# Kernel tuning notes

Measured on AMD Instinct MI355X. Metric: run time of the kernel, lower is better.

Reference implementation:

```python
import jax, jax.numpy as jnp
import numpy as np

EPS = 1e-5
B, CIN, L = 512, 5, 1024   # batch, input channels, msp length == d_model
COUT, A, NB = 32, 13, 5    # CNN branch channels, max_atoms, num_bonds_prediction


def conv1d(x, w, pad, groups=1):
    # x: (N, C, L), w: (O, I/groups, K)
    return jax.lax.conv_general_dilated(
        x, w, window_strides=(1,), padding=[(pad, pad)],
        dimension_numbers=("NCH", "OIH", "NCH"), feature_group_count=groups)


def batchnorm(x, g, b):
    # training-mode BN over (N, L) per channel, as nn.BatchNorm1d in train()
    m = jnp.mean(x, axis=(0, 2), keepdims=True)
    v = jnp.var(x, axis=(0, 2), keepdims=True)
    return (x - m) * jax.lax.rsqrt(v + EPS) * g[None, :, None] + b[None, :, None]


def setup_inputs() -> dict:
    key = jax.random.key(0)
    ks = jax.random.split(key, 16)
    n = jax.random.normal
    inp = {
        "src": n(ks[0], (B, CIN, L), dtype=jnp.float32),
        "mask": jnp.ones((B, A), dtype=bool),
        "max_atoms": A,
        # CNN branch 1 (kernel 5) : depthwise, pointwise, BN, residual 1x1 conv
        "dw1": n(ks[1], (CIN, 1, 5), dtype=jnp.float32) * 0.2,
        "pw1": n(ks[2], (COUT, CIN, 1), dtype=jnp.float32) * 0.2,
        "g1": jnp.ones((COUT,), jnp.float32),
        "be1": jnp.zeros((COUT,), jnp.float32),
        "r1w": n(ks[3], (COUT, CIN, 1), dtype=jnp.float32) * 0.2,
        "r1b": jnp.zeros((COUT,), jnp.float32),
        # CNN branch 2 (kernel 3)
        "dw2": n(ks[4], (CIN, 1, 3), dtype=jnp.float32) * 0.2,
        "pw2": n(ks[5], (COUT, CIN, 1), dtype=jnp.float32) * 0.2,
        "g2": jnp.ones((COUT,), jnp.float32),
        "be2": jnp.zeros((COUT,), jnp.float32),
        "r2w": n(ks[6], (COUT, CIN, 1), dtype=jnp.float32) * 0.2,
        "r2b": jnp.zeros((COUT,), jnp.float32),
        # EdgeClassify2 linears: ll1 (2*COUT -> A), fl (2*L -> NB)
        "ll1w": n(ks[7], (A, 2 * COUT), dtype=jnp.float32) * 0.1,
        "ll1b": jnp.zeros((A,), jnp.float32),
        "flw": n(ks[8], (NB, 2 * L), dtype=jnp.float32) * 0.02,
        "flb": jnp.zeros((NB,), jnp.float32),
    }
    return inp


def reference(src, mask, max_atoms, dw1, pw1, g1, be1, r1w, r1b,
              dw2, pw2, g2, be2, r2w, r2b, ll1w, ll1b, flw, flb):
    # ---- CNN encoder ----
    e1 = jax.nn.relu(batchnorm(conv1d(conv1d(src, dw1, 2, groups=CIN), pw1, 0), g1, be1))
    e1 = e1 * (conv1d(src, r1w, 0) + r1b[None, :, None])
    e2 = jax.nn.relu(batchnorm(conv1d(conv1d(src, dw2, 1, groups=CIN), pw2, 0), g2, be2))
    e2 = e2 * (conv1d(src, r2w, 0) + r2b[None, :, None])
    x = jnp.concatenate([e1, e2], axis=1)          # (B, 2*COUT, L)
    # ---- EdgeClassify2 ----
    # ll1 over channel dim: (B, 2*COUT, L) -> (B, A, L)
    h = jnp.einsum("bcl,ac->bal", x, ll1w) + ll1b[None, :, None]
    # vectorized replacement of the O(A^2) python loop:
    # final_e[:, i, j] = concat(h[:, min(i,j)], h[:, max(i,j)])
    idx = jnp.arange(max_atoms)
    mn = jnp.minimum(idx[:, None], idx[None, :])   # (A, A)
    mx = jnp.maximum(idx[:, None], idx[None, :])
    final_e = jnp.concatenate([h[:, mn, :], h[:, mx, :]], axis=-1)  # (B, A, A, 2L)
    out = jnp.einsum("bijd,nd->bijn", final_e, flw) + flb           # (B, A, A, NB)
    return out
```

## Files before the change

kernel.cpp:

```cpp
#include <hip/hip_runtime.h>
#include <hip/hip_bf16.h>

#define BB 512
#define LL 1024
#define AA 13
#define NBP 5
#define NTOT (BB * LL)
#define EPSV 1e-5f

#define WS_F     192
#define WS_PART  256
#define WS_CONST 10496

typedef __attribute__((ext_vector_type(8))) short bhalf8;
typedef __attribute__((ext_vector_type(4))) float floatx4;

template<int CTRL, int RM, bool BC>
__device__ __forceinline__ float dppadd(float v) {
    int t = __builtin_amdgcn_update_dpp(0, __float_as_int(v), CTRL, RM, 0xf, BC);
    return v + __int_as_float(t);
}
__device__ __forceinline__ float wave_sum(float v) {
    v = dppadd<0x111, 0xf, true >(v);
    v = dppadd<0x112, 0xf, true >(v);
    v = dppadd<0x114, 0xf, true >(v);
    v = dppadd<0x118, 0xf, true >(v);
    v = dppadd<0x142, 0xa, false>(v);
    v = dppadd<0x143, 0xc, false>(v);
    return v;
}

__global__ __launch_bounds__(256) void k_moments(
    const float* __restrict__ src,
    const float* __restrict__ dw1,
    const float* __restrict__ dw2,
    const float* __restrict__ flw,
    float* __restrict__ ws)
{
    __shared__ float red[4][40];
    __shared__ float fred[4];
    int tid = threadIdx.x;
    int gid = blockIdx.x * 256 + tid;
    int b = gid >> 7, L0 = (gid & 127) << 3;
    const float* sb = src + b * (5 * LL);

    float w1[5][5], w2[5][3];
#pragma unroll
    for (int c = 0; c < 5; c++) {
#pragma unroll
        for (int t = 0; t < 5; t++) w1[c][t] = dw1[c*5+t];
#pragma unroll
        for (int t = 0; t < 3; t++) w2[c][t] = dw2[c*3+t];
    }

    float x[5][16];
#pragma unroll
    for (int c5 = 0; c5 < 5; c5++) {
        const float* sp = sb + c5 * LL;
        float4 xa = (L0 >= 4)    ? *(const float4*)(sp + L0 - 4) : make_float4(0,0,0,0);
        float4 xb = *(const float4*)(sp + L0);
        float4 xc = *(const float4*)(sp + L0 + 4);
        float4 xd = (L0 <= 1012) ? *(const float4*)(sp + L0 + 8) : make_float4(0,0,0,0);
        x[c5][0]=xa.x; x[c5][1]=xa.y; x[c5][2]=xa.z; x[c5][3]=xa.w;
        x[c5][4]=xb.x; x[c5][5]=xb.y; x[c5][6]=xb.z; x[c5][7]=xb.w;
        x[c5][8]=xc.x; x[c5][9]=xc.y; x[c5][10]=xc.z; x[c5][11]=xc.w;
        x[c5][12]=xd.x; x[c5][13]=xd.y; x[c5][14]=xd.z; x[c5][15]=xd.w;
    }

    float acc[40];
#pragma unroll
    for (int k = 0; k < 40; k++) acc[k] = 0.f;

#pragma unroll
    for (int k = 0; k < 8; k++) {
        float d1[5], d2[5];
#pragma unroll
        for (int c5 = 0; c5 < 5; c5++) {
            d1[c5] = w1[c5][0]*x[c5][k+2] + w1[c5][1]*x[c5][k+3] + w1[c5][2]*x[c5][k+4]
                   + w1[c5][3]*x[c5][k+5] + w1[c5][4]*x[c5][k+6];
            d2[c5] = w2[c5][0]*x[c5][k+3] + w2[c5][1]*x[c5][k+4] + w2[c5][2]*x[c5][k+5];
        }
#pragma unroll
        for (int j = 0; j < 5; j++) { acc[j] += d1[j]; acc[20+j] += d2[j]; }
#pragma unroll
        for (int j = 0; j < 5; j++)
#pragma unroll
            for (int kk = j; kk < 5; kk++) {
                int idx = j*(11-j)/2 + (kk - j);
                acc[5+idx]  += d1[j]*d1[kk];
                acc[25+idx] += d2[j]*d2[kk];
            }
    }

    int lane = tid & 63, wv = tid >> 6;
#pragma unroll
    for (int k = 0; k < 40; k++) acc[k] = wave_sum(acc[k]);
    if (lane == 63) {
#pragma unroll
        for (int k = 0; k < 40; k++) red[wv][k] = acc[k];
    }
    __syncthreads();
    if (tid < 40) {
        ws[WS_PART + blockIdx.x * 40 + tid] =
            red[0][tid] + red[1][tid] + red[2][tid] + red[3][tid];
    }

    if (blockIdx.x < 10) {
        int nn = blockIdx.x;
        int n = nn < 5 ? nn : nn - 5;
        int off = nn < 5 ? 0 : LL;
        float4 v = *(const float4*)(flw + n * (2*LL) + off + tid * 4);
        float s = wave_sum(v.x + v.y + v.z + v.w);
        if (lane == 63) fred[wv] = s;
        __syncthreads();
        if (tid == 0) ws[WS_F + nn] = fred[0] + fred[1] + fred[2] + fred[3];
    }
}

__global__ __launch_bounds__(320) void k_prep(
    float* __restrict__ ws,
    const float* __restrict__ pw1, const float* __restrict__ pw2,
    const float* __restrict__ g1,  const float* __restrict__ be1,
    const float* __restrict__ g2,  const float* __restrict__ be2,
    const float* __restrict__ r1w, const float* __restrict__ r2w,
    const float* __restrict__ r1b, const float* __restrict__ r2b)
{
    __shared__ float momS[40];
    int tid = threadIdx.x;
    {
        int k = tid >> 3, sub = tid & 7;
        float v = 0.f;
#pragma unroll 8
        for (int t2 = 0; t2 < 32; t2++) v += ws[WS_PART + (sub + (t2 << 3)) * 40 + k];
        v += __shfl_xor(v, 1, 64);
        v += __shfl_xor(v, 2, 64);
        v += __shfl_xor(v, 4, 64);
        if (sub == 0) momS[k] = v;
    }
    __syncthreads();
    if (tid < 64) {
        int brc = tid >> 5, o = tid & 31;
        const float invN = 1.0f / (float)NTOT;
        const float* pw = brc ? pw2 : pw1;
        const float* rw = brc ? r2w : r1w;
        const float* s  = momS + (brc ? 20 : 0);
        const float* M  = momS + (brc ? 25 : 5);
        float pwv[5], rwv[5], md[5];
#pragma unroll
        for (int j = 0; j < 5; j++) { pwv[j] = pw[o*5+j]; rwv[j] = rw[o*5+j]; md[j] = s[j] * invN; }
        float meanY = 0.f;
#pragma unroll
        for (int j = 0; j < 5; j++) meanY += pwv[j] * md[j];
        float ey2 = 0.f;
#pragma unroll
        for (int j = 0; j < 5; j++)
#pragma unroll
            for (int k = 0; k < 5; k++) {
                int lo = j < k ? j : k, hi = j < k ? k : j;
                int idx = lo*(11-lo)/2 + (hi - lo);
                ey2 += pwv[j] * pwv[k] * (M[idx] * invN);
            }
        float varY = ey2 - meanY * meanY;
        if (varY < 0.f) varY = 0.f;
        float gg = brc ? g2[o] : g1[o];
        float bb = brc ? be2[o] : be1[o];
        float rb = brc ? r2b[o] : r1b[o];
        float sc = gg * rsqrtf(varY + EPSV);
        float sh = bb - meanY * sc;
        float* dst = ws + WS_CONST + tid * 16;
        dst[0] = pwv[0]*sc; dst[1] = pwv[1]*sc; dst[2] = pwv[2]*sc; dst[3] = pwv[3]*sc;
        dst[4] = pwv[4]*sc; dst[5] = sh;        dst[6] = rb;        dst[7] = 0.f;
        dst[8] = rwv[0];    dst[9] = rwv[1];    dst[10] = rwv[2];   dst[11] = rwv[3];
        dst[12] = rwv[4];   dst[13] = 0.f;      dst[14] = 0.f;      dst[15] = 0.f;
    }
}

__global__ __launch_bounds__(1024, 1) void k_fused(
    const float* __restrict__ src,
    const float* __restrict__ dw1,
    const float* __restrict__ dw2,
    const float* __restrict__ flw,
    const float* __restrict__ ll1w,
    const float* __restrict__ ll1b,
    const float* __restrict__ flb,
    const float* __restrict__ ws,
    float* __restrict__ out)
{
    __shared__ __align__(16) float srcS[5][1040];
    __shared__ float llT[832];
    __shared__ __align__(16) unsigned int eBuf[16384];
    __shared__ __align__(16) float Sarr[1024];
    __shared__ float PQ[130];

    int tid = threadIdx.x, b = blockIdx.x;
    int lane = tid & 63;
    int gu = __builtin_amdgcn_readfirstlane(tid >> 6);
    int br = gu >> 3;
    int c0 = gu << 2;

    const float* srcB = src + b * (5 * LL);

    for (int idx = tid; idx < 5 * 256; idx += 1024) {
        int c5 = idx >> 8, q = idx & 255;
        float4 v = *(const float4*)(srcB + (c5 << 10) + (q << 2));
        *(float4*)&srcS[c5][(q << 2) + 8] = v;
    }
    if (tid < 40) {
        int c5 = tid >> 3, j = tid & 7;
        int i = (j < 4) ? (4 + j) : (1028 + j);
        srcS[c5][i] = 0.f;
    }
    for (int idx = tid; idx < 832; idx += 1024) {
        int cc = idx / 13, a = idx - cc * 13;
        llT[idx] = ll1w[a * 64 + cc];
    }

    float wdw[5][5];
    if (br == 0) {
#pragma unroll
        for (int c5 = 0; c5 < 5; c5++)
#pragma unroll
            for (int t = 0; t < 5; t++) wdw[c5][t] = dw1[c5*5+t];
    } else {
#pragma unroll
        for (int c5 = 0; c5 < 5; c5++) {
            wdw[c5][0] = 0.f;
            wdw[c5][1] = dw2[c5*3+0]; wdw[c5][2] = dw2[c5*3+1]; wdw[c5][3] = dw2[c5*3+2];
            wdw[c5][4] = 0.f;
        }
    }
    const float* cb = ws + WS_CONST + (c0 << 4);

    int mt  = gu & 3;
    int ks0 = (gu >> 2) << 1;
    floatx4 Cacc = {0.f, 0.f, 0.f, 0.f};

    int nB = lane & 15;
    int kg = (lane >> 4) << 3;
    const float* fbase = flw + (nB % 5) * 2048 + (nB / 5) * 1024;

    __syncthreads();

#pragma unroll 1
    for (int p = 0; p < 4; ++p) {
        float fv[2][8];
        {
            int gl0 = (p << 8) + (ks0 << 5) + kg;
            if (nB < 10) {
                float4 a0 = *(const float4*)(fbase + gl0);
                float4 a1 = *(const float4*)(fbase + gl0 + 4);
                float4 b0 = *(const float4*)(fbase + gl0 + 32);
                float4 b1 = *(const float4*)(fbase + gl0 + 36);
                fv[0][0]=a0.x; fv[0][1]=a0.y; fv[0][2]=a0.z; fv[0][3]=a0.w;
                fv[0][4]=a1.x; fv[0][5]=a1.y; fv[0][6]=a1.z; fv[0][7]=a1.w;
                fv[1][0]=b0.x; fv[1][1]=b0.y; fv[1][2]=b0.z; fv[1][3]=b0.w;
                fv[1][4]=b1.x; fv[1][5]=b1.y; fv[1][6]=b1.z; fv[1][7]=b1.w;
            } else {
#pragma unroll
                for (int j = 0; j < 8; j++) { fv[0][j] = 0.f; fv[1][j] = 0.f; }
            }
        }

        int l0 = (p << 8) + (lane << 2);
        float dv[5][4], sv[5][4];
        {
            int i0 = l0 + 8;
#pragma unroll
            for (int c5 = 0; c5 < 5; c5++) {
                float4 xa = *(const float4*)&srcS[c5][i0 - 4];
                float4 xb = *(const float4*)&srcS[c5][i0];
                float4 xc = *(const float4*)&srcS[c5][i0 + 4];
                float xx[12] = {xa.x, xa.y, xa.z, xa.w, xb.x, xb.y, xb.z, xb.w, xc.x, xc.y, xc.z, xc.w};
                sv[c5][0] = xb.x; sv[c5][1] = xb.y; sv[c5][2] = xb.z; sv[c5][3] = xb.w;
                if (br == 0) {
#pragma unroll
                    for (int q = 0; q < 4; q++)
                        dv[c5][q] = wdw[c5][0]*xx[q+2] + wdw[c5][1]*xx[q+3] + wdw[c5][2]*xx[q+4]
                                  + wdw[c5][3]*xx[q+5] + wdw[c5][4]*xx[q+6];
                } else {
#pragma unroll
                    for (int q = 0; q < 4; q++)
                        dv[c5][q] = wdw[c5][1]*xx[q+3] + wdw[c5][2]*xx[q+4] + wdw[c5][3]*xx[q+5];
                }
            }
        }

        char* eb = (char*)eBuf;
#pragma unroll
        for (int ci = 0; ci < 4; ci++) {
            const float4 A  = *(const float4*)(cb + ci*16);
            const float4 B2 = *(const float4*)(cb + ci*16 + 4);
            const float4 R0 = *(const float4*)(cb + ci*16 + 8);
            const float4 R1 = *(const float4*)(cb + ci*16 + 12);
            unsigned int hp[2], lp[2];
#pragma unroll
            for (int hq = 0; hq < 2; hq++) {
                unsigned int hw[2], lw[2];
#pragma unroll
                for (int s = 0; s < 2; s++) {
                    int q = hq * 2 + s;
                    float y = B2.y + A.x*dv[0][q] + A.y*dv[1][q] + A.z*dv[2][q]
                                    + A.w*dv[3][q] + B2.x*dv[4][q];
                    float r = B2.z + R0.x*sv[0][q] + R0.y*sv[1][q] + R0.z*sv[2][q]
                                    + R0.w*sv[3][q] + R1.x*sv[4][q];
                    float e = fmaxf(y, 0.f) * r;
                    unsigned int u = __float_as_uint(e);
                    hw[s] = u & 0xFFFF0000u;
                    float lf = e - __uint_as_float(hw[s]);
                    lw[s] = __float_as_uint(lf) & 0xFFFF0000u;
                }
                hp[hq] = (hw[0] >> 16) | hw[1];
                lp[hq] = (lw[0] >> 16) | lw[1];
            }
            int c = c0 + ci;
            int off = (c << 9) + (((lane << 3)) ^ ((c & 7) << 4));
            *(uint2*)(eb + off)         = make_uint2(hp[0], hp[1]);
            *(uint2*)(eb + 32768 + off) = make_uint2(lp[0], lp[1]);
        }
        __syncthreads();

        {
            int arow = (mt << 4) + (lane & 15);
            int swz  = (arow & 7) << 4;
            int rb2  = arow << 9;
#pragma unroll
            for (int kk = 0; kk < 2; kk++) {
                int ksl = (ks0 + kk) << 5;
                int kbyte = (((ksl + kg) << 1)) ^ swz;
                bhalf8 aH = *(const bhalf8*)(eb + rb2 + kbyte);
                bhalf8 aL = *(const bhalf8*)(eb + 32768 + rb2 + kbyte);
                bhalf8 bH, bL;
#pragma unroll
                for (int j = 0; j < 8; j++) {
                    float f = fv[kk][j];
                    unsigned int u = __float_as_uint(f);
                    unsigned int hu = u & 0xFFFF0000u;
                    bH[j] = (short)(u >> 16);
                    float lf = f - __uint_as_float(hu);
                    bL[j] = (short)(__float_as_uint(lf) >> 16);
                }
                Cacc = __builtin_amdgcn_mfma_f32_16x16x32_bf16(aH, bH, Cacc, 0, 0, 0);
                Cacc = __builtin_amdgcn_mfma_f32_16x16x32_bf16(aH, bL, Cacc, 0, 0, 0);
                Cacc = __builtin_amdgcn_mfma_f32_16x16x32_bf16(aL, bH, Cacc, 0, 0, 0);
            }
        }
        __syncthreads();
    }

    {
        float* part = (float*)eBuf;
        int basep = (gu << 8) + ((lane >> 4) << 6) + (lane & 15);
        part[basep]      = Cacc[0];
        part[basep + 16] = Cacc[1];
        part[basep + 32] = Cacc[2];
        part[basep + 48] = Cacc[3];
    }
    __syncthreads();
    {
        int c = tid >> 4, n = tid & 15;
        int m = c >> 4, row = c & 15;
        const float* part = (const float*)eBuf;
        int o = (row << 4) + n;
        float s = part[(m) * 256 + o] + part[(4 + m) * 256 + o]
                + part[(8 + m) * 256 + o] + part[(12 + m) * 256 + o];
        Sarr[tid] = s;
    }
    __syncthreads();

    if (tid < 130) {
        int half = tid >= 65 ? 1 : 0;
        int q = tid - half * 65;
        int a = q / 5, n = q - a * 5;
        int col = half * 5 + n;
        float v = ll1b[a] * ws[WS_F + col];
#pragma unroll 8
        for (int cc = 0; cc < 64; cc++) v += llT[cc * 13 + a] * Sarr[(cc << 4) + col];
        PQ[tid] = v;
    }
    __syncthreads();

    for (int idx = tid; idx < AA * AA * NBP; idx += 1024) {
        int i = idx / 65;
        int rr = idx - i * 65;
        int j = rr / 5, n = rr - j * 5;
        int mn = i < j ? i : j, mx = i < j ? j : i;
        out[b * (AA * AA * NBP) + idx] = PQ[mn * 5 + n] + PQ[65 + mx * 5 + n] + flb[n];
    }
}

extern "C" void kernel_launch(void* const* d_in, const int* in_sizes, int n_in,
                              void* d_out, int out_size, void* d_ws, size_t ws_size,
                              hipStream_t stream) {
    const float* src  = (const float*)d_in[0];
    const float* dw1  = (const float*)d_in[3];
    const float* pw1  = (const float*)d_in[4];
    const float* g1   = (const float*)d_in[5];
    const float* be1  = (const float*)d_in[6];
    const float* r1w  = (const float*)d_in[7];
    const float* r1b  = (const float*)d_in[8];
    const float* dw2  = (const float*)d_in[9];
    const float* pw2  = (const float*)d_in[10];
    const float* g2   = (const float*)d_in[11];
    const float* be2  = (const float*)d_in[12];
    const float* r2w  = (const float*)d_in[13];
    const float* r2b  = (const float*)d_in[14];
    const float* ll1w = (const float*)d_in[15];
    const float* ll1b = (const float*)d_in[16];
    const float* flw  = (const float*)d_in[17];
    const float* flb  = (const float*)d_in[18];
    float* ws  = (float*)d_ws;
    float* out = (float*)d_out;

    k_moments<<<256, 256, 0, stream>>>(src, dw1, dw2, flw, ws);
    k_prep<<<1, 320, 0, stream>>>(ws, pw1, pw2, g1, be1, g2, be2, r1w, r2w, r1b, r2b);
    k_fused<<<BB, 1024, 0, stream>>>(src, dw1, dw2, flw, ll1w, ll1b, flb, ws, out);
}
```

Measured before the change: 142.4 us.

## Halve shared eBuf by staging hi/lo bf16 halves sequentially for two blocks per CU

The shared staging buffer for the split-bf16 activation tile is halved. The high part is written first and consumed by two MFMAs, then the low part is held in registers, written into the same buffer and consumed by the third MFMA. Launch bounds are raised to allow two 1024-thread blocks per CU. The aim is to cut LDS use so a second block can hide latency. The cost is two extra __syncthreads per iteration and more register pressure under a tighter register budget.

```diff
diff --git a/kernel.cpp b/kernel.cpp
--- a/kernel.cpp
+++ b/kernel.cpp
@@ -175,7 +175,7 @@
     }
 }
 
-__global__ __launch_bounds__(1024, 1) void k_fused(
+__global__ __launch_bounds__(1024, 2) void k_fused(
     const float* __restrict__ src,
     const float* __restrict__ dw1,
     const float* __restrict__ dw2,
@@ -188,7 +188,7 @@
 {
     __shared__ __align__(16) float srcS[5][1040];
     __shared__ float llT[832];
-    __shared__ __align__(16) unsigned int eBuf[16384];
+    __shared__ __align__(16) unsigned int eBuf[8192];
     __shared__ __align__(16) float Sarr[1024];
     __shared__ float PQ[130];
 
@@ -286,6 +286,7 @@
         }
 
         char* eb = (char*)eBuf;
+        unsigned int lpK[8];
 #pragma unroll
         for (int ci = 0; ci < 4; ci++) {
             const float4 A  = *(const float4*)(cb + ci*16);
@@ -313,36 +314,54 @@
                 lp[hq] = (lw[0] >> 16) | lw[1];
             }
             int c = c0 + ci;
-            int off = (c << 9) + (((lane << 3)) ^ ((c & 7) << 4));
-            *(uint2*)(eb + off)         = make_uint2(hp[0], hp[1]);
-            *(uint2*)(eb + 32768 + off) = make_uint2(lp[0], lp[1]);
+            int off = (c << 9) + ((lane << 3) ^ ((c & 7) << 4));
+            *(uint2*)(eb + off) = make_uint2(hp[0], hp[1]);
+            lpK[ci*2]   = lp[0];
+            lpK[ci*2+1] = lp[1];
         }
         __syncthreads();
 
-        {
-            int arow = (mt << 4) + (lane & 15);
-            int swz  = (arow & 7) << 4;
-            int rb2  = arow << 9;
-#pragma unroll
-            for (int kk = 0; kk < 2; kk++) {
-                int ksl = (ks0 + kk) << 5;
-                int kbyte = (((ksl + kg) << 1)) ^ swz;
-                bhalf8 aH = *(const bhalf8*)(eb + rb2 + kbyte);
-                bhalf8 aL = *(const bhalf8*)(eb + 32768 + rb2 + kbyte);
-                bhalf8 bH, bL;
-#pragma unroll
-                for (int j = 0; j < 8; j++) {
-                    float f = fv[kk][j];
-                    unsigned int u = __float_as_uint(f);
-                    unsigned int hu = u & 0xFFFF0000u;
-                    bH[j] = (short)(u >> 16);
-                    float lf = f - __uint_as_float(hu);
-                    bL[j] = (short)(__float_as_uint(lf) >> 16);
-                }
-                Cacc = __builtin_amdgcn_mfma_f32_16x16x32_bf16(aH, bH, Cacc, 0, 0, 0);
-                Cacc = __builtin_amdgcn_mfma_f32_16x16x32_bf16(aH, bL, Cacc, 0, 0, 0);
-                Cacc = __builtin_amdgcn_mfma_f32_16x16x32_bf16(aL, bH, Cacc, 0, 0, 0);
-            }
+        bhalf8 bH[2], bL[2];
+#pragma unroll
+        for (int kk = 0; kk < 2; kk++) {
+#pragma unroll
+            for (int j = 0; j < 8; j++) {
+                float f = fv[kk][j];
+                unsigned int u = __float_as_uint(f);
+                unsigned int hu = u & 0xFFFF0000u;
+                bH[kk][j] = (short)(u >> 16);
+                float lf = f - __uint_as_float(hu);
+                bL[kk][j] = (short)(__float_as_uint(lf) >> 16);
+            }
+        }
+
+        int arow = (mt << 4) + (lane & 15);
+        int swz  = (arow & 7) << 4;
+        int rb2  = arow << 9;
+#pragma unroll
+        for (int kk = 0; kk < 2; kk++) {
+            int ksl = (ks0 + kk) << 5;
+            int kbyte = ((ksl + kg) << 1) ^ swz;
+            bhalf8 aH = *(const bhalf8*)(eb + rb2 + kbyte);
+            Cacc = __builtin_amdgcn_mfma_f32_16x16x32_bf16(aH, bH[kk], Cacc, 0, 0, 0);
+            Cacc = __builtin_amdgcn_mfma_f32_16x16x32_bf16(aH, bL[kk], Cacc, 0, 0, 0);
+        }
+        __syncthreads();
+
+#pragma unroll
+        for (int ci = 0; ci < 4; ci++) {
+            int c = c0 + ci;
+            int off = (c << 9) + ((lane << 3) ^ ((c & 7) << 4));
+            *(uint2*)(eb + off) = make_uint2(lpK[ci*2], lpK[ci*2+1]);
+        }
+        __syncthreads();
+
+#pragma unroll
+        for (int kk = 0; kk < 2; kk++) {
+            int ksl = (ks0 + kk) << 5;
+            int kbyte = ((ksl + kg) << 1) ^ swz;
+            bhalf8 aL = *(const bhalf8*)(eb + rb2 + kbyte);
+            Cacc = __builtin_amdgcn_mfma_f32_16x16x32_bf16(aL, bH[kk], Cacc, 0, 0, 0);
         }
         __syncthreads();
     }
```

New measurement: 142.7 us. No clear change (+0.2%).

## Shrink fused block to 512 threads and read src directly from global

Applied to the files above, without the earlier changes.

The fused kernel drops from 1024 to 512 threads per block, with each wave handling 8 channels instead of 4 and the sequence processed in 8 chunks of 128 instead of 4 of 256. The shared src staging buffer is removed: the depthwise convolution now reads src straight from global memory with boundary checks. Sarr and PQ are aliased onto the shrunken eBuf. Together these cut shared memory per block so up to 4 blocks can share a CU, aiming at better occupancy and latency hiding. The cost is redundant, less coalesced global loads of src and more loop iterations and barriers per block.

```diff
diff --git a/kernel.cpp b/kernel.cpp
--- a/kernel.cpp
+++ b/kernel.cpp
@@ -175,7 +175,7 @@
     }
 }
 
-__global__ __launch_bounds__(1024, 1) void k_fused(
+__global__ __launch_bounds__(512, 4) void k_fused(
     const float* __restrict__ src,
     const float* __restrict__ dw1,
     const float* __restrict__ dw2,
@@ -186,31 +186,18 @@
     const float* __restrict__ ws,
     float* __restrict__ out)
 {
-    __shared__ __align__(16) float srcS[5][1040];
     __shared__ float llT[832];
-    __shared__ __align__(16) unsigned int eBuf[16384];
-    __shared__ __align__(16) float Sarr[1024];
-    __shared__ float PQ[130];
+    __shared__ __align__(16) unsigned int eBuf[8192];
 
     int tid = threadIdx.x, b = blockIdx.x;
     int lane = tid & 63;
     int gu = __builtin_amdgcn_readfirstlane(tid >> 6);
-    int br = gu >> 3;
-    int c0 = gu << 2;
+    int br = gu >> 2;
+    int c0 = gu << 3;
 
     const float* srcB = src + b * (5 * LL);
 
-    for (int idx = tid; idx < 5 * 256; idx += 1024) {
-        int c5 = idx >> 8, q = idx & 255;
-        float4 v = *(const float4*)(srcB + (c5 << 10) + (q << 2));
-        *(float4*)&srcS[c5][(q << 2) + 8] = v;
-    }
-    if (tid < 40) {
-        int c5 = tid >> 3, j = tid & 7;
-        int i = (j < 4) ? (4 + j) : (1028 + j);
-        srcS[c5][i] = 0.f;
-    }
-    for (int idx = tid; idx < 832; idx += 1024) {
+    for (int idx = tid; idx < 832; idx += 512) {
         int cc = idx / 13, a = idx - cc * 13;
         llT[idx] = ll1w[a * 64 + cc];
     }
@@ -231,21 +218,21 @@
     }
     const float* cb = ws + WS_CONST + (c0 << 4);
 
-    int mt  = gu & 3;
-    int ks0 = (gu >> 2) << 1;
+    int mt   = gu & 3;
+    int kgrp = gu >> 2;
     floatx4 Cacc = {0.f, 0.f, 0.f, 0.f};
 
     int nB = lane & 15;
     int kg = (lane >> 4) << 3;
     const float* fbase = flw + (nB % 5) * 2048 + (nB / 5) * 1024;
 
-    __syncthreads();
+    char* eb = (char*)eBuf;
 
 #pragma unroll 1
-    for (int p = 0; p < 4; ++p) {
+    for (int p = 0; p < 8; ++p) {
         float fv[2][8];
         {
-            int gl0 = (p << 8) + (ks0 << 5) + kg;
+            int gl0 = (p << 7) + (kgrp << 6) + kg;
             if (nB < 10) {
                 float4 a0 = *(const float4*)(fbase + gl0);
                 float4 a1 = *(const float4*)(fbase + gl0 + 4);
@@ -261,87 +248,78 @@
             }
         }
 
-        int l0 = (p << 8) + (lane << 2);
-        float dv[5][4], sv[5][4];
-        {
-            int i0 = l0 + 8;
-#pragma unroll
-            for (int c5 = 0; c5 < 5; c5++) {
-                float4 xa = *(const float4*)&srcS[c5][i0 - 4];
-                float4 xb = *(const float4*)&srcS[c5][i0];
-                float4 xc = *(const float4*)&srcS[c5][i0 + 4];
-                float xx[12] = {xa.x, xa.y, xa.z, xa.w, xb.x, xb.y, xb.z, xb.w, xc.x, xc.y, xc.z, xc.w};
-                sv[c5][0] = xb.x; sv[c5][1] = xb.y; sv[c5][2] = xb.z; sv[c5][3] = xb.w;
-                if (br == 0) {
-#pragma unroll
-                    for (int q = 0; q < 4; q++)
-                        dv[c5][q] = wdw[c5][0]*xx[q+2] + wdw[c5][1]*xx[q+3] + wdw[c5][2]*xx[q+4]
-                                  + wdw[c5][3]*xx[q+5] + wdw[c5][4]*xx[q+6];
-                } else {
-#pragma unroll
-                    for (int q = 0; q < 4; q++)
-                        dv[c5][q] = wdw[c5][1]*xx[q+3] + wdw[c5][2]*xx[q+4] + wdw[c5][3]*xx[q+5];
-                }
-            }
-        }
-
-        char* eb = (char*)eBuf;
-#pragma unroll
-        for (int ci = 0; ci < 4; ci++) {
+        int l0 = (p << 7) + (lane << 1);
+        float dv[5][2], sv[5][2];
+#pragma unroll
+        for (int c5 = 0; c5 < 5; c5++) {
+            const float* s5 = srcB + (c5 << 10);
+            float2 xa = (l0 >= 2)    ? *(const float2*)(s5 + l0 - 2) : make_float2(0.f, 0.f);
+            float2 xb = *(const float2*)(s5 + l0);
+            float2 xc = (l0 <= 1020) ? *(const float2*)(s5 + l0 + 2) : make_float2(0.f, 0.f);
+            float xx[6] = {xa.x, xa.y, xb.x, xb.y, xc.x, xc.y};
+            sv[c5][0] = xb.x; sv[c5][1] = xb.y;
+            if (br == 0) {
+#pragma unroll
+                for (int q = 0; q < 2; q++)
+                    dv[c5][q] = wdw[c5][0]*xx[q] + wdw[c5][1]*xx[q+1] + wdw[c5][2]*xx[q+2]
+                              + wdw[c5][3]*xx[q+3] + wdw[c5][4]*xx[q+4];
+            } else {
+#pragma unroll
+                for (int q = 0; q < 2; q++)
+                    dv[c5][q] = wdw[c5][1]*xx[q+1] + wdw[c5][2]*xx[q+2] + wdw[c5][3]*xx[q+3];
+            }
+        }
+
+        int wcol = lane << 2;
+#pragma unroll
+        for (int ci = 0; ci < 8; ci++) {
             const float4 A  = *(const float4*)(cb + ci*16);
             const float4 B2 = *(const float4*)(cb + ci*16 + 4);
             const float4 R0 = *(const float4*)(cb + ci*16 + 8);
             const float4 R1 = *(const float4*)(cb + ci*16 + 12);
-            unsigned int hp[2], lp[2];
-#pragma unroll
-            for (int hq = 0; hq < 2; hq++) {
-                unsigned int hw[2], lw[2];
-#pragma unroll
-                for (int s = 0; s < 2; s++) {
-                    int q = hq * 2 + s;
-                    float y = B2.y + A.x*dv[0][q] + A.y*dv[1][q] + A.z*dv[2][q]
-                                    + A.w*dv[3][q] + B2.x*dv[4][q];
-                    float r = B2.z + R0.x*sv[0][q] + R0.y*sv[1][q] + R0.z*sv[2][q]
-                                    + R0.w*sv[3][q] + R1.x*sv[4][q];
-                    float e = fmaxf(y, 0.f) * r;
-                    unsigned int u = __float_as_uint(e);
-                    hw[s] = u & 0xFFFF0000u;
-                    float lf = e - __uint_as_float(hw[s]);
-                    lw[s] = __float_as_uint(lf) & 0xFFFF0000u;
-                }
-                hp[hq] = (hw[0] >> 16) | hw[1];
-                lp[hq] = (lw[0] >> 16) | lw[1];
+            unsigned int hw[2], lw[2];
+#pragma unroll
+            for (int q = 0; q < 2; q++) {
+                float y = B2.y + A.x*dv[0][q] + A.y*dv[1][q] + A.z*dv[2][q]
+                                + A.w*dv[3][q] + B2.x*dv[4][q];
+                float r = B2.z + R0.x*sv[0][q] + R0.y*sv[1][q] + R0.z*sv[2][q]
+                                + R0.w*sv[3][q] + R1.x*sv[4][q];
+                float e = fmaxf(y, 0.f) * r;
+                unsigned int u = __float_as_uint(e);
+                hw[q] = u & 0xFFFF0000u;
+                float lf = e - __uint_as_float(hw[q]);
+                lw[q] = __float_as_uint(lf) & 0xFFFF0000u;
             }
             int c = c0 + ci;
-            int off = (c << 9) + (((lane << 3)) ^ ((c & 7) << 4));
-            *(uint2*)(eb + off)         = make_uint2(hp[0], hp[1]);
-            *(uint2*)(eb + 32768 + off) = make_uint2(lp[0], lp[1]);
+            int off = (c << 8) + (wcol ^ ((c & 7) << 4));
+            *(unsigned int*)(eb + off)         = (hw[0] >> 16) | hw[1];
+            *(unsigned int*)(eb + 16384 + off) = (lw[0] >> 16) | lw[1];
         }
         __syncthreads();
 
         {
             int arow = (mt << 4) + (lane & 15);
             int swz  = (arow & 7) << 4;
-            int rb2  = arow << 9;
-#pragma unroll
-            for (int kk = 0; kk < 2; kk++) {
-                int ksl = (ks0 + kk) << 5;
-                int kbyte = (((ksl + kg) << 1)) ^ swz;
-                bhalf8 aH = *(const bhalf8*)(eb + rb2 + kbyte);
-                bhalf8 aL = *(const bhalf8*)(eb + 32768 + rb2 + kbyte);
-                bhalf8 bH, bL;
+            int rb2  = arow << 8;
+            bhalf8 bH[2], bL[2];
+#pragma unroll
+            for (int kk = 0; kk < 2; kk++)
 #pragma unroll
                 for (int j = 0; j < 8; j++) {
                     float f = fv[kk][j];
                     unsigned int u = __float_as_uint(f);
-                    unsigned int hu = u & 0xFFFF0000u;
-                    bH[j] = (short)(u >> 16);
-                    float lf = f - __uint_as_float(hu);
-                    bL[j] = (short)(__float_as_uint(lf) >> 16);
+                    bH[kk][j] = (short)(u >> 16);
+                    float lf = f - __uint_as_float(u & 0xFFFF0000u);
+                    bL[kk][j] = (short)(__float_as_uint(lf) >> 16);
                 }
-                Cacc = __builtin_amdgcn_mfma_f32_16x16x32_bf16(aH, bH, Cacc, 0, 0, 0);
-                Cacc = __builtin_amdgcn_mfma_f32_16x16x32_bf16(aH, bL, Cacc, 0, 0, 0);
-                Cacc = __builtin_amdgcn_mfma_f32_16x16x32_bf16(aL, bH, Cacc, 0, 0, 0);
+#pragma unroll
+            for (int kk = 0; kk < 2; kk++) {
+                int kbyte = (((kgrp << 6) + (kk << 5) + kg) << 1) ^ swz;
+                bhalf8 aH = *(const bhalf8*)(eb + rb2 + kbyte);
+                bhalf8 aL = *(const bhalf8*)(eb + 16384 + rb2 + kbyte);
+                Cacc = __builtin_amdgcn_mfma_f32_16x16x32_bf16(aH, bH[kk], Cacc, 0, 0, 0);
+                Cacc = __builtin_amdgcn_mfma_f32_16x16x32_bf16(aH, bL[kk], Cacc, 0, 0, 0);
+                Cacc = __builtin_amdgcn_mfma_f32_16x16x32_bf16(aL, bH[kk], Cacc, 0, 0, 0);
             }
         }
         __syncthreads();
@@ -356,17 +334,17 @@
         part[basep + 48] = Cacc[3];
     }
     __syncthreads();
-    {
-        int c = tid >> 4, n = tid & 15;
-        int m = c >> 4, row = c & 15;
+    float* SarrF = (float*)eBuf + 4096;
+    for (int idx = tid; idx < 1024; idx += 512) {
+        int c = idx >> 4, n = idx & 15;
+        int mt2 = c >> 4, row = c & 15;
         const float* part = (const float*)eBuf;
         int o = (row << 4) + n;
-        float s = part[(m) * 256 + o] + part[(4 + m) * 256 + o]
-                + part[(8 + m) * 256 + o] + part[(12 + m) * 256 + o];
-        Sarr[tid] = s;
-    }
-    __syncthreads();
-
+        SarrF[idx] = part[mt2 * 256 + o] + part[(4 + mt2) * 256 + o];
+    }
+    __syncthreads();
+
+    float* PQ = (float*)eBuf + 5120;
     if (tid < 130) {
         int half = tid >= 65 ? 1 : 0;
         int q = tid - half * 65;
@@ -374,12 +352,12 @@
         int col = half * 5 + n;
         float v = ll1b[a] * ws[WS_F + col];
 #pragma unroll 8
-        for (int cc = 0; cc < 64; cc++) v += llT[cc * 13 + a] * Sarr[(cc << 4) + col];
+        for (int cc = 0; cc < 64; cc++) v += llT[cc * 13 + a] * SarrF[(cc << 4) + col];
         PQ[tid] = v;
     }
     __syncthreads();
 
-    for (int idx = tid; idx < AA * AA * NBP; idx += 1024) {
+    for (int idx = tid; idx < AA * AA * NBP; idx += 512) {
         int i = idx / 65;
         int rr = idx - i * 65;
         int j = rr / 5, n = rr - j * 5;
@@ -413,5 +391,5 @@
 
     k_moments<<<256, 256, 0, stream>>>(src, dw1, dw2, flw, ws);
     k_prep<<<1, 320, 0, stream>>>(ws, pw1, pw2, g1, be1, g2, be2, r1w, r2w, r1b, r2b);
-    k_fused<<<BB, 1024, 0, stream>>>(src, dw1, dw2, flw, ll1w, ll1b, flb, ws, out);
-}
+    k_fused<<<BB, 512, 0, stream>>>(src, dw1, dw2, flw, ll1w, ll1b, flb, ws, out);
+}
```

New measurement: 153.0 us. 7.4% more time.
